# Performance work log

Measured on AMD Instinct MI355X. Metric: run time of the kernel, lower is better.

## Reference

```python
import jax, jax.numpy as jnp
import numpy as np


def setup_inputs() -> dict:
    key = jax.random.key(0)
    k1, k2, k3, k4 = jax.random.split(key, 4)
    B, S, H, D = 4, 2048, 1024, 1024
    X = jax.random.normal(k1, (B, S, H), dtype=jnp.float32)
    # nn.Linear weight stored as [out, in]; we store as [in, out] for x @ W
    scale = 1.0 / np.sqrt(H)
    Wq = jax.random.normal(k2, (H, D), dtype=jnp.float32) * scale
    Wk = jax.random.normal(k3, (H, D), dtype=jnp.float32) * scale
    Wv = jax.random.normal(k4, (H, D), dtype=jnp.float32) * scale
    return {"X": X, "Wq": Wq, "Wk": Wk, "Wv": Wv}


def reference(X, Wq, Wk, Wv):
    B, S, H = X.shape
    q = X @ Wq  # [B, S, D]
    k = X @ Wk
    v = X @ Wv
    D = k.shape[-1]
    scores = jnp.einsum('bqd,bkd->bqk', q, k) / jnp.sqrt(jnp.float32(D))
    causal = jnp.tril(jnp.ones((S, S), dtype=bool))  # block_size mask sliced to S
    scores = jnp.where(causal, scores, -jnp.inf)
    weights = jax.nn.softmax(scores, axis=-1)  # dropout p=0.0 -> identity
    return jnp.einsum('bqk,bkd->bqd', weights, v)
```

## Files before the change

### kernel.cpp

```cpp
#include <hip/hip_runtime.h>

#define AS1 __attribute__((address_space(1)))
#define AS3 __attribute__((address_space(3)))

typedef __attribute__((ext_vector_type(8))) short short8;
typedef __attribute__((ext_vector_type(4))) float floatx4;

__device__ __forceinline__ short f2bf(float f) {
  union { float f; unsigned u; } v; v.f = f;
  return (short)((v.u + 0x7fffu + ((v.u >> 16) & 1u)) >> 16);
}
__device__ __forceinline__ float bf2f(short s) {
  union { unsigned u; float f; } v; v.u = ((unsigned)(unsigned short)s) << 16;
  return v.f;
}

__device__ __forceinline__ void gload_lds16(const void* g, void* l) {
  __builtin_amdgcn_global_load_lds((const AS1 unsigned*)g, (AS3 unsigned*)l, 16, 0, 0);
}

__device__ __forceinline__ void stage128x64(const short* __restrict__ G, long rowBase, long ld,
                                            int kBase, short* lds, int lane, int wave) {
  const short* gb = G + rowBase * ld + (long)kBase + (long)(lane >> 3) * ld + (lane & 7) * 8;
#pragma unroll
  for (int j = 0; j < 4; ++j) {
    int c = wave * 4 + j;
    gload_lds16(gb + (long)c * 8 * ld, lds + c * 512);
  }
}

__device__ __forceinline__ void mfma_step(const short* lA, const short* lB, floatx4 acc[4][4],
                                          int lane, int wm, int wn) {
#pragma unroll
  for (int kk = 0; kk < 64; kk += 32) {
    short8 a[4], b[4];
    int kq = kk + (lane >> 4) * 8;
#pragma unroll
    for (int i = 0; i < 4; ++i) {
      a[i] = *(const short8*)(lA + (wm * 64 + i * 16 + (lane & 15)) * 64 + kq);
      b[i] = *(const short8*)(lB + (wn * 64 + i * 16 + (lane & 15)) * 64 + kq);
    }
#pragma unroll
    for (int i = 0; i < 4; ++i)
#pragma unroll
      for (int j = 0; j < 4; ++j)
        acc[i][j] = __builtin_amdgcn_mfma_f32_16x16x32_bf16(a[i], b[j], acc[i][j], 0, 0, 0);
  }
}

__global__ void convert_x(const float* __restrict__ X, short* __restrict__ Xb, long n) {
  long stride = (long)gridDim.x * blockDim.x * 4;
  for (long i = ((long)blockIdx.x * blockDim.x + threadIdx.x) * 4; i < n; i += stride) {
    float4 v = *(const float4*)(X + i);
    short4 o;
    o.x = f2bf(v.x); o.y = f2bf(v.y); o.z = f2bf(v.z); o.w = f2bf(v.w);
    *(short4*)(Xb + i) = o;
  }
}

__global__ void transpose_w(const float* __restrict__ Wq, const float* __restrict__ Wk,
                            const float* __restrict__ Wv, short* __restrict__ Wt) {
  __shared__ float t[32][33];
  const float* W = blockIdx.z == 0 ? Wq : (blockIdx.z == 1 ? Wk : Wv);
  short* O = Wt + (long)blockIdx.z * 1024 * 1024;
  int x = blockIdx.x * 32 + threadIdx.x;
  int y0 = blockIdx.y * 32;
  for (int j = threadIdx.y; j < 32; j += 8)
    t[j][threadIdx.x] = W[(long)(y0 + j) * 1024 + x];
  __syncthreads();
  int x2 = blockIdx.y * 32 + threadIdx.x;
  int y2 = blockIdx.x * 32;
  for (int j = threadIdx.y; j < 32; j += 8)
    O[(long)(y2 + j) * 1024 + x2] = f2bf(t[threadIdx.x][j]);
}

__global__ __launch_bounds__(256, 3) void gemm_qkv(const short* __restrict__ Xb,
                                                   const short* __restrict__ Wt,
                                                   short* __restrict__ Q, short* __restrict__ K2,
                                                   short* __restrict__ Vt) {
  __shared__ short lA[128 * 64], lB[128 * 64];
  const int lane = threadIdx.x & 63, wave = threadIdx.x >> 6;
  const int wm = wave >> 1, wn = wave & 1;
  const int z = blockIdx.z;
  const short* Bm = Wt + (long)z * 1024 * 1024;
  const long mBase = (long)blockIdx.x * 128;
  const long nBase = (long)blockIdx.y * 128;

  floatx4 acc[4][4];
  const floatx4 zero = {0.f, 0.f, 0.f, 0.f};
#pragma unroll
  for (int i = 0; i < 4; ++i)
#pragma unroll
    for (int j = 0; j < 4; ++j) acc[i][j] = zero;

  for (int kt = 0; kt < 16; ++kt) {
    stage128x64(Xb, mBase, 1024, kt * 64, lA, lane, wave);
    stage128x64(Bm, nBase, 1024, kt * 64, lB, lane, wave);
    __syncthreads();
    mfma_step(lA, lB, acc, lane, wm, wn);
    __syncthreads();
  }

  if (z < 2) {
    short* out = (z == 0) ? Q : K2;
#pragma unroll
    for (int i = 0; i < 4; ++i)
#pragma unroll
      for (int j = 0; j < 4; ++j) {
        int col = (int)nBase + wn * 64 + j * 16 + (lane & 15);
#pragma unroll
        for (int r = 0; r < 4; ++r) {
          long m = mBase + wm * 64 + i * 16 + (lane >> 4) * 4 + r;
          out[m * 1024 + col] = f2bf(acc[i][j][r]);
        }
      }
  } else {
    const long bb = mBase >> 11;
    const int sBase = (int)(mBase & 2047);
#pragma unroll
    for (int i = 0; i < 4; ++i) {
      int s0 = sBase + wm * 64 + i * 16 + ((lane >> 4) << 2);
#pragma unroll
      for (int j = 0; j < 4; ++j) {
        int col = (int)nBase + wn * 64 + j * 16 + (lane & 15);
        short4 o;
        o.x = f2bf(acc[i][j][0]); o.y = f2bf(acc[i][j][1]);
        o.z = f2bf(acc[i][j][2]); o.w = f2bf(acc[i][j][3]);
        *(short4*)(Vt + ((bb * 1024 + col) * 2048 + s0)) = o;
      }
    }
  }
}

__global__ __launch_bounds__(256, 3) void scores_exp(const short* __restrict__ Q,
                                                     const short* __restrict__ Kk,
                                                     short* __restrict__ E, float* __restrict__ l) {
  __shared__ short lA[128 * 64], lB[128 * 64];
  const int lane = threadIdx.x & 63, wave = threadIdx.x >> 6;
  const int wm = wave >> 1, wn = wave & 1;
  const int b = blockIdx.y;
  int qt = 0, rem = blockIdx.x;
  while (rem > qt) { rem -= (qt + 1); ++qt; }
  const int kt = rem;

  const long rowQ = (long)b * 2048 + (long)qt * 128;
  const long rowK = (long)b * 2048 + (long)kt * 128;

  floatx4 acc[4][4];
  const floatx4 zero = {0.f, 0.f, 0.f, 0.f};
#pragma unroll
  for (int i = 0; i < 4; ++i)
#pragma unroll
    for (int j = 0; j < 4; ++j) acc[i][j] = zero;

  for (int it = 0; it < 16; ++it) {
    stage128x64(Q, rowQ, 1024, it * 64, lA, lane, wave);
    stage128x64(Kk, rowK, 1024, it * 64, lB, lane, wave);
    __syncthreads();
    mfma_step(lA, lB, acc, lane, wm, wn);
    __syncthreads();
  }

  short* Eb = E + (long)b * 2048 * 2048;
  float* lrow = l + (long)b * 2048;
#pragma unroll
  for (int i = 0; i < 4; ++i) {
#pragma unroll
    for (int r = 0; r < 4; ++r) {
      int ri = wm * 64 + i * 16 + (lane >> 4) * 4 + r;
      int qrow = qt * 128 + ri;
      float p = 0.f;
#pragma unroll
      for (int j = 0; j < 4; ++j) {
        int col = kt * 128 + wn * 64 + j * 16 + (lane & 15);
        float s = acc[i][j][r] * 0.03125f;
        float e = (col <= qrow) ? __expf(s) : 0.0f;
        short eb = f2bf(e);
        Eb[(long)qrow * 2048 + col] = eb;
        p += bf2f(eb);
      }
      for (int m = 1; m < 16; m <<= 1) p += __shfl_xor(p, m, 64);
      if ((lane & 15) == 0) atomicAdd(&lrow[qrow], p);
    }
  }
}

__global__ __launch_bounds__(256, 3) void pv_gemm(const short* __restrict__ E,
                                                  const short* __restrict__ Vt,
                                                  const float* __restrict__ l,
                                                  float* __restrict__ out) {
  __shared__ short lA[128 * 64], lB[128 * 64];
  const int lane = threadIdx.x & 63, wave = threadIdx.x >> 6;
  const int wm = wave >> 1, wn = wave & 1;
  const int qt = 15 - blockIdx.x, dt = blockIdx.y, b = blockIdx.z;
  const short* Eb = E + (long)b * 2048 * 2048;
  const short* Vb = Vt + (long)b * 1024 * 2048;
  const float* lrow = l + (long)b * 2048;

  floatx4 acc[4][4];
  const floatx4 zero = {0.f, 0.f, 0.f, 0.f};
#pragma unroll
  for (int i = 0; i < 4; ++i)
#pragma unroll
    for (int j = 0; j < 4; ++j) acc[i][j] = zero;

  const int nIter = (qt + 1) * 2;
  for (int it = 0; it < nIter; ++it) {
    stage128x64(Eb, (long)qt * 128, 2048, it * 64, lA, lane, wave);
    stage128x64(Vb, (long)dt * 128, 2048, it * 64, lB, lane, wave);
    __syncthreads();
    mfma_step(lA, lB, acc, lane, wm, wn);
    __syncthreads();
  }

#pragma unroll
  for (int i = 0; i < 4; ++i) {
#pragma unroll
    for (int r = 0; r < 4; ++r) {
      int qrow = qt * 128 + wm * 64 + i * 16 + (lane >> 4) * 4 + r;
      float inv = 1.0f / lrow[qrow];
#pragma unroll
      for (int j = 0; j < 4; ++j) {
        int d = dt * 128 + wn * 64 + j * 16 + (lane & 15);
        out[((long)b * 2048 + qrow) * 1024 + d] = acc[i][j][r] * inv;
      }
    }
  }
}

extern "C" void kernel_launch(void* const* d_in, const int* in_sizes, int n_in,
                              void* d_out, int out_size, void* d_ws, size_t ws_size,
                              hipStream_t stream) {
  const float* X  = (const float*)d_in[0];
  const float* Wq = (const float*)d_in[1];
  const float* Wk = (const float*)d_in[2];
  const float* Wv = (const float*)d_in[3];

  char* ws = (char*)d_ws;
  short* Xb = (short*)(ws);
  short* Wt = (short*)(ws + 16777216L);
  short* Q  = (short*)(ws + 23068672L);
  short* K2 = (short*)(ws + 39845888L);
  short* Vt = (short*)(ws + 56623104L);
  short* E  = (short*)(ws + 73400320L);
  float* l  = (float*)(ws + 106954752L);

  hipMemsetAsync(l, 0, 4 * 2048 * sizeof(float), stream);
  convert_x<<<2048, 256, 0, stream>>>(X, Xb, 8192L * 1024);
  transpose_w<<<dim3(32, 32, 3), dim3(32, 8), 0, stream>>>(Wq, Wk, Wv, Wt);
  gemm_qkv<<<dim3(64, 8, 3), 256, 0, stream>>>(Xb, Wt, Q, K2, Vt);
  scores_exp<<<dim3(136, 4), 256, 0, stream>>>(Q, K2, E, l);
  pv_gemm<<<dim3(16, 8, 4), 256, 0, stream>>>(E, Vt, l, (float*)d_out);
}
```

Before: 249.5 us.

## Split long causal PV tiles across two blocks and fuse input prep kernels

The P·V GEMM splits the K range of the eight heaviest causal query tiles across two blocks. One block writes its partial sum directly to the output and the other writes to a scratch buffer, then a new reduce kernel adds the two halves and applies the softmax normalization. This targets the load imbalance of the triangular work distribution. Separately, the X conversion and weight transpose are merged into one launch to save a kernel launch. The cost is an extra reduce pass and partial-buffer traffic, and the scratch buffer reuses the Xb workspace region.

```diff
diff --git a/kernel.cpp b/kernel.cpp
--- a/kernel.cpp
+++ b/kernel.cpp
@@ -48,30 +48,33 @@
   }
 }
 
-__global__ void convert_x(const float* __restrict__ X, short* __restrict__ Xb, long n) {
-  long stride = (long)gridDim.x * blockDim.x * 4;
-  for (long i = ((long)blockIdx.x * blockDim.x + threadIdx.x) * 4; i < n; i += stride) {
+__global__ void prep_inputs(const float* __restrict__ X, const float* __restrict__ Wq,
+                            const float* __restrict__ Wk, const float* __restrict__ Wv,
+                            short* __restrict__ Xb, short* __restrict__ Wt) {
+  __shared__ float t[32][33];
+  if (blockIdx.x < 8192) {
+    long i = ((long)blockIdx.x * 256 + threadIdx.x) * 4;
     float4 v = *(const float4*)(X + i);
     short4 o;
     o.x = f2bf(v.x); o.y = f2bf(v.y); o.z = f2bf(v.z); o.w = f2bf(v.w);
     *(short4*)(Xb + i) = o;
-  }
-}
-
-__global__ void transpose_w(const float* __restrict__ Wq, const float* __restrict__ Wk,
-                            const float* __restrict__ Wv, short* __restrict__ Wt) {
-  __shared__ float t[32][33];
-  const float* W = blockIdx.z == 0 ? Wq : (blockIdx.z == 1 ? Wk : Wv);
-  short* O = Wt + (long)blockIdx.z * 1024 * 1024;
-  int x = blockIdx.x * 32 + threadIdx.x;
-  int y0 = blockIdx.y * 32;
-  for (int j = threadIdx.y; j < 32; j += 8)
-    t[j][threadIdx.x] = W[(long)(y0 + j) * 1024 + x];
-  __syncthreads();
-  int x2 = blockIdx.y * 32 + threadIdx.x;
-  int y2 = blockIdx.x * 32;
-  for (int j = threadIdx.y; j < 32; j += 8)
-    O[(long)(y2 + j) * 1024 + x2] = f2bf(t[threadIdx.x][j]);
+  } else {
+    int idx = blockIdx.x - 8192;
+    int z = idx >> 10, rem = idx & 1023;
+    int bx = rem >> 5, by = rem & 31;
+    const float* W = z == 0 ? Wq : (z == 1 ? Wk : Wv);
+    short* O = Wt + (long)z * 1024 * 1024;
+    int tx = threadIdx.x & 31, ty = threadIdx.x >> 5;
+    int x = bx * 32 + tx;
+    int y0 = by * 32;
+    for (int j = ty; j < 32; j += 8)
+      t[j][tx] = W[(long)(y0 + j) * 1024 + x];
+    __syncthreads();
+    int x2 = by * 32 + tx;
+    int y2 = bx * 32;
+    for (int j = ty; j < 32; j += 8)
+      O[(long)(y2 + j) * 1024 + x2] = f2bf(t[tx][j]);
+  }
 }
 
 __global__ __launch_bounds__(256, 3) void gemm_qkv(const short* __restrict__ Xb,
@@ -188,11 +191,23 @@
 __global__ __launch_bounds__(256, 3) void pv_gemm(const short* __restrict__ E,
                                                   const short* __restrict__ Vt,
                                                   const float* __restrict__ l,
+                                                  float* __restrict__ part,
                                                   float* __restrict__ out) {
   __shared__ short lA[128 * 64], lB[128 * 64];
   const int lane = threadIdx.x & 63, wave = threadIdx.x >> 6;
   const int wm = wave >> 1, wn = wave & 1;
-  const int qt = 15 - blockIdx.x, dt = blockIdx.y, b = blockIdx.z;
+  const int x = blockIdx.x, dt = blockIdx.y, b = blockIdx.z;
+
+  int qt, it0, it1, mode;
+  if (x < 16) {
+    qt = 8 + (x >> 1);
+    const int T = (qt + 1) * 2, c0 = T >> 1;
+    if ((x & 1) == 0) { it0 = 0; it1 = c0; mode = 1; }
+    else              { it0 = c0; it1 = T; mode = 2; }
+  } else {
+    qt = x - 16; it0 = 0; it1 = (qt + 1) * 2; mode = 0;
+  }
+
   const short* Eb = E + (long)b * 2048 * 2048;
   const short* Vb = Vt + (long)b * 1024 * 2048;
   const float* lrow = l + (long)b * 2048;
@@ -204,8 +219,7 @@
 #pragma unroll
     for (int j = 0; j < 4; ++j) acc[i][j] = zero;
 
-  const int nIter = (qt + 1) * 2;
-  for (int it = 0; it < nIter; ++it) {
+  for (int it = it0; it < it1; ++it) {
     stage128x64(Eb, (long)qt * 128, 2048, it * 64, lA, lane, wave);
     stage128x64(Vb, (long)dt * 128, 2048, it * 64, lB, lane, wave);
     __syncthreads();
@@ -213,19 +227,50 @@
     __syncthreads();
   }
 
-#pragma unroll
-  for (int i = 0; i < 4; ++i) {
-#pragma unroll
-    for (int r = 0; r < 4; ++r) {
-      int qrow = qt * 128 + wm * 64 + i * 16 + (lane >> 4) * 4 + r;
-      float inv = 1.0f / lrow[qrow];
-#pragma unroll
-      for (int j = 0; j < 4; ++j) {
-        int d = dt * 128 + wn * 64 + j * 16 + (lane & 15);
-        out[((long)b * 2048 + qrow) * 1024 + d] = acc[i][j][r] * inv;
-      }
-    }
-  }
+  if (mode == 2) {
+    float* P = part + ((((long)b * 8 + (qt - 8)) * 8 + dt) << 14);
+#pragma unroll
+    for (int i = 0; i < 4; ++i)
+#pragma unroll
+      for (int r = 0; r < 4; ++r) {
+        int ri = wm * 64 + i * 16 + (lane >> 4) * 4 + r;
+#pragma unroll
+        for (int j = 0; j < 4; ++j) {
+          int ci = wn * 64 + j * 16 + (lane & 15);
+          P[ri * 128 + ci] = acc[i][j][r];
+        }
+      }
+  } else {
+#pragma unroll
+    for (int i = 0; i < 4; ++i)
+#pragma unroll
+      for (int r = 0; r < 4; ++r) {
+        int qrow = qt * 128 + wm * 64 + i * 16 + (lane >> 4) * 4 + r;
+        float scale = (mode == 0) ? 1.0f / lrow[qrow] : 1.0f;
+#pragma unroll
+        for (int j = 0; j < 4; ++j) {
+          int d = dt * 128 + wn * 64 + j * 16 + (lane & 15);
+          out[((long)b * 2048 + qrow) * 1024 + d] = acc[i][j][r] * scale;
+        }
+      }
+  }
+}
+
+__global__ void pv_reduce(float* __restrict__ out, const float* __restrict__ part,
+                          const float* __restrict__ l) {
+  const int idx = blockIdx.x;
+  const int b = idx >> 10;
+  const int row = 1024 + (idx & 1023);
+  const int t = threadIdx.x;
+  const int dt = t >> 5, dl = (t << 2) & 127;
+  const float inv = 1.0f / l[((long)b << 11) + row];
+  const long pbase = ((((long)b * 8 + ((row >> 7) - 8)) * 8 + dt) << 14) + ((row & 127) << 7) + dl;
+  const long obase = (((long)b * 2048 + row) << 10) + (t << 2);
+  float4 o = *(const float4*)(out + obase);
+  float4 p = *(const float4*)(part + pbase);
+  o.x = (o.x + p.x) * inv; o.y = (o.y + p.y) * inv;
+  o.z = (o.z + p.z) * inv; o.w = (o.w + p.w) * inv;
+  *(float4*)(out + obase) = o;
 }
 
 extern "C" void kernel_launch(void* const* d_in, const int* in_sizes, int n_in,
@@ -244,11 +289,12 @@
   short* Vt = (short*)(ws + 56623104L);
   short* E  = (short*)(ws + 73400320L);
   float* l  = (float*)(ws + 106954752L);
+  float* part = (float*)(ws);
 
   hipMemsetAsync(l, 0, 4 * 2048 * sizeof(float), stream);
-  convert_x<<<2048, 256, 0, stream>>>(X, Xb, 8192L * 1024);
-  transpose_w<<<dim3(32, 32, 3), dim3(32, 8), 0, stream>>>(Wq, Wk, Wv, Wt);
+  prep_inputs<<<11264, 256, 0, stream>>>(X, Wq, Wk, Wv, Xb, Wt);
   gemm_qkv<<<dim3(64, 8, 3), 256, 0, stream>>>(Xb, Wt, Q, K2, Vt);
   scores_exp<<<dim3(136, 4), 256, 0, stream>>>(Q, K2, E, l);
-  pv_gemm<<<dim3(16, 8, 4), 256, 0, stream>>>(E, Vt, l, (float*)d_out);
-}
+  pv_gemm<<<dim3(24, 8, 4), 256, 0, stream>>>(E, Vt, l, part, (float*)d_out);
+  pv_reduce<<<4096, 256, 0, stream>>>((float*)d_out, part, l);
+}
```

Measured after the change: 244.1 us. 2.1% less time.
